# Optimization experiments

Measured on AMD Instinct MI355X. Metric: run time of the kernel, lower is better.

## Reference

```python
import jax, jax.numpy as jnp
import numpy as np

N_SRC, N_TGT, N_EDGES = 100000, 50000, 600000
IN_CH, OUT_CH = 128, 128
NUM_EDGE_TYPES, NUM_NODE_TYPES = 7, 4


def setup_inputs() -> dict:
    key = jax.random.key(0)
    ks = jax.random.split(key, 9)
    x_src = jax.random.normal(ks[0], (N_SRC, IN_CH), dtype=jnp.float32)
    x_target = jax.random.normal(ks[1], (N_TGT, IN_CH), dtype=jnp.float32)
    # PyG Linear: y = x @ W.T (+ b); W has shape (out, in)
    rel_w = jax.random.normal(ks[2], (NUM_EDGE_TYPES, OUT_CH, IN_CH), dtype=jnp.float32) * 0.05
    root_w = jax.random.normal(ks[3], (NUM_NODE_TYPES, OUT_CH, IN_CH), dtype=jnp.float32) * 0.05
    root_b = jax.random.normal(ks[4], (NUM_NODE_TYPES, OUT_CH), dtype=jnp.float32) * 0.05
    edge_src = jax.random.randint(ks[5], (N_EDGES,), 0, N_SRC, dtype=jnp.int32)
    edge_dst = jax.random.randint(ks[6], (N_EDGES,), 0, N_TGT, dtype=jnp.int32)
    edge_type = jax.random.randint(ks[7], (N_EDGES,), 0, NUM_EDGE_TYPES, dtype=jnp.int32)
    target_node_type = jax.random.randint(ks[8], (N_TGT,), 0, NUM_NODE_TYPES, dtype=jnp.int32)
    return {
        "x_src": x_src, "x_target": x_target,
        "rel_w": rel_w, "root_w": root_w, "root_b": root_b,
        "edge_src": edge_src, "edge_dst": edge_dst,
        "edge_type": edge_type, "target_node_type": target_node_type,
    }


def reference(x_src, x_target, rel_w, root_w, root_b,
              edge_src, edge_dst, edge_type, target_node_type):
    n_tgt = x_target.shape[0]
    num_rel = rel_w.shape[0]
    num_ntypes = root_w.shape[0]
    # Gather source features once for all edges: (E, in)
    msg = x_src[edge_src]
    out = jnp.zeros((n_tgt, rel_w.shape[1]), dtype=x_target.dtype)
    # Per-relation linear transform + scatter-MEAN over that relation's edges
    # (matches one propagate(aggr='mean') call per edge type: nodes with no
    #  incoming edges of type r contribute 0 for that relation).
    for r in range(num_rel):
        mask = (edge_type == r).astype(msg.dtype)  # (E,)
        y = (msg * mask[:, None]) @ rel_w[r].T     # (E, out)
        s = jax.ops.segment_sum(y, edge_dst, num_segments=n_tgt)
        cnt = jax.ops.segment_sum(mask, edge_dst, num_segments=n_tgt)
        out = out + s / jnp.maximum(cnt, 1.0)[:, None]
    # Per-node-type root linear (with bias), masked add
    for t in range(num_ntypes):
        m = (target_node_type == t)
        root = x_target @ root_w[t].T + root_b[t]
        out = out + jnp.where(m[:, None], root, 0.0)
    return out
```

## Files before the change

### kernel.cpp

```cpp
#include <hip/hip_runtime.h>

#define NSRC 100000
#define NTGT 50000
#define NE   600000
#define CH   128
#define NREL 7
#define NTYP 4
#define NP   (NREL * NTGT)
#define NB   ((NP + 1023) / 1024)
#define NBLK ((NTGT + 31) / 32)

typedef __attribute__((ext_vector_type(4))) float f32x4;
typedef __attribute__((ext_vector_type(8))) short bf16x8;
typedef unsigned int uint;
typedef unsigned short ushort;

static constexpr long long NXT4 = (long long)NTGT * CH / 4;
static constexpr long long NWR4 = (long long)NREL * CH * CH / 4;
static constexpr long long NWT4 = (long long)NTYP * CH * CH / 4;
static constexpr int CONVB  = (int)((NXT4 + NWR4 + NWT4 + 255) / 256);
static constexpr int COUNTB = (NE + 255) / 256;
static constexpr int GATB   = NE / 16;

static constexpr size_t A256(size_t x) { return (x + 255) & ~(size_t)255; }
static constexpr size_t CNT_O   = 0;
static constexpr size_t BSE_O   = A256(CNT_O + (size_t)NP * 4);
static constexpr size_t EOFF_O  = A256(BSE_O + (size_t)NB * 4);
static constexpr size_t CUR_O   = A256(EOFF_O + (size_t)(NP + 1) * 4);
static constexpr size_t WB_O    = A256(CUR_O + (size_t)NP * 4);
static constexpr size_t XTB_O   = A256(WB_O + (size_t)(NREL + NTYP) * CH * CH * 2);
static constexpr size_t MSG_O   = A256(XTB_O + (size_t)NTGT * CH * 2);

#define GLOAD_LDS(gp, lp) __builtin_amdgcn_global_load_lds( \
    (const __attribute__((address_space(1))) void*)(gp), \
    (__attribute__((address_space(3))) void*)(lp), 16, 0, 0)
#define WAITVM4()   asm volatile("s_waitcnt vmcnt(4)" ::: "memory")
#define WAITVM0()   asm volatile("s_waitcnt vmcnt(0)" ::: "memory")
#define WAITLGKM0() asm volatile("s_waitcnt lgkmcnt(0)" ::: "memory")

__device__ __forceinline__ uint bfpack(float a, float b) {
  uint ua = __float_as_uint(a); ua = (ua + 0x7fff + ((ua >> 16) & 1)) >> 16;
  uint ub = __float_as_uint(b); ub = (ub + 0x7fff + ((ub >> 16) & 1)) >> 16;
  return ua | (ub << 16);
}
__device__ __forceinline__ ushort f2b(float x) {
  uint u = __float_as_uint(x);
  return (ushort)((u + 0x7fff + ((u >> 16) & 1)) >> 16);
}
__device__ __forceinline__ float bl(uint u) { return __uint_as_float(u << 16); }
__device__ __forceinline__ float bh(uint u) { return __uint_as_float(u & 0xffff0000u); }

__global__ __launch_bounds__(256) void k_pre(
    const float* __restrict__ xt, const float* __restrict__ relw,
    const float* __restrict__ rootw, ushort* __restrict__ xtb,
    ushort* __restrict__ wb,
    const int* __restrict__ edst, const int* __restrict__ etyp,
    int* __restrict__ cnt) {
  int bx = blockIdx.x;
  if (bx < CONVB) {
    long long i4 = (long long)bx * 256 + threadIdx.x;
    const float* src; ushort* dst; long long off;
    if (i4 < NXT4) { src = xt; dst = xtb; off = i4; }
    else if (i4 < NXT4 + NWR4) { src = relw; dst = wb; off = i4 - NXT4; }
    else if (i4 < NXT4 + NWR4 + NWT4) {
      src = rootw; dst = wb + (size_t)NREL * CH * CH; off = i4 - NXT4 - NWR4;
    } else return;
    float4 v = *(const float4*)(src + off * 4);
    uint lo = (uint)f2b(v.x) | ((uint)f2b(v.y) << 16);
    uint hi = (uint)f2b(v.z) | ((uint)f2b(v.w) << 16);
    uint2 o = make_uint2(lo, hi);
    *(uint2*)(dst + off * 4) = o;
    return;
  }
  bx -= CONVB;
  int i = bx * 256 + threadIdx.x;
  if (i < NE) atomicAdd(&cnt[etyp[i] * NTGT + edst[i]], 1);
}

__global__ __launch_bounds__(256) void k_s1(const int* __restrict__ cnt,
                                            int* __restrict__ bsE) {
  __shared__ int sE[256];
  int t = threadIdx.x, p0 = blockIdx.x * 1024 + t * 4;
  int e = 0;
#pragma unroll
  for (int j = 0; j < 4; ++j) {
    int p = p0 + j;
    if (p < NP) e += cnt[p];
  }
  sE[t] = e; __syncthreads();
  for (int s = 128; s > 0; s >>= 1) {
    if (t < s) sE[t] += sE[t + s];
    __syncthreads();
  }
  if (t == 0) bsE[blockIdx.x] = sE[0];
}

__global__ __launch_bounds__(512) void k_s23(const int* __restrict__ cnt,
                                             const int* __restrict__ bsE,
                                             int* __restrict__ eoff,
                                             int* __restrict__ cur) {
  __shared__ int sE[512];
  __shared__ int sBase;
  int t = threadIdx.x;
  int e = (t < NB) ? bsE[t] : 0;
  sE[t] = e; __syncthreads();
  for (int s = 1; s < 512; s <<= 1) {
    int a = 0; if (t >= s) a = sE[t - s];
    __syncthreads();
    sE[t] += a;
    __syncthreads();
  }
  if (t == blockIdx.x) sBase = sE[t] - e;
  __syncthreads();
  int base0 = sBase;
  int p0 = blockIdx.x * 1024 + t * 2;
  int c0 = (p0 < NP) ? cnt[p0] : 0;
  int c1 = (p0 + 1 < NP) ? cnt[p0 + 1] : 0;
  int e2 = c0 + c1;
  sE[t] = e2; __syncthreads();
  for (int s = 1; s < 512; s <<= 1) {
    int a = 0; if (t >= s) a = sE[t - s];
    __syncthreads();
    sE[t] += a;
    __syncthreads();
  }
  int baseE = base0 + sE[t] - e2;
  if (p0 < NP)     { eoff[p0] = baseE;          cur[p0] = baseE; }
  if (p0 + 1 < NP) { eoff[p0 + 1] = baseE + c0; cur[p0 + 1] = baseE + c0; }
  if (p0 + 1 == NP - 1) eoff[NP] = baseE + c0 + c1;
}

__global__ __launch_bounds__(256) void k_gat(
    const float* __restrict__ xsrc, const int* __restrict__ esrc,
    const int* __restrict__ edst, const int* __restrict__ etyp,
    int* __restrict__ cur, ushort* __restrict__ msg) {
  int tid = threadIdx.x;
  int e = blockIdx.x * 16 + (tid >> 4);
  int l16 = tid & 15;
  int src = esrc[e];
  int p = etyp[e] * NTGT + edst[e];
  int pos = 0;
  if (l16 == 0) pos = atomicAdd(&cur[p], 1);
  pos = __shfl(pos, (tid & 63) & ~15);
  const float* rp = xsrc + (size_t)src * CH + l16 * 8;
  float4 v0 = *(const float4*)rp;
  float4 v1 = *(const float4*)(rp + 4);
  uint4 o;
  o.x = bfpack(v0.x, v0.y); o.y = bfpack(v0.z, v0.w);
  o.z = bfpack(v1.x, v1.y); o.w = bfpack(v1.z, v1.w);
  *(uint4*)(msg + (size_t)pos * CH + l16 * 8) = o;
}

__device__ __forceinline__ void mfma_acc(const ushort* strip, const ushort* W,
                                         int m, int quad, f32x4* acc) {
  bf16x8 aF[4];
#pragma unroll
  for (int ks = 0; ks < 4; ++ks) {
    int c = ks * 4 + quad;
    aF[ks] = *(const bf16x8*)&strip[(m * 16 + (c ^ m)) << 3];
  }
#pragma unroll
  for (int ct = 0; ct < 8; ++ct) {
    int n = ct * 16 + m;
#pragma unroll
    for (int ks = 0; ks < 4; ++ks) {
      bf16x8 bF = *(const bf16x8*)(W + (size_t)n * CH + ks * 32 + quad * 8);
      acc[ct] = __builtin_amdgcn_mfma_f32_16x16x32_bf16(aF[ks], bF, acc[ct], 0, 0, 0);
    }
  }
}

__global__ __launch_bounds__(128) void k_mega(const ushort* __restrict__ msg,
    const ushort* __restrict__ xtb, const ushort* __restrict__ wb,
    const int* __restrict__ eoff, const int* __restrict__ ntyp,
    const float* __restrict__ rootb, float* __restrict__ out) {
  __shared__ ushort As[2 * 6144];
  int wv = threadIdx.x >> 6, ln = threadIdx.x & 63;
  ushort* Wbuf = As + wv * 6144;
  ushort* strip = Wbuf + 4096;
  int m = ln & 15, quad = ln >> 4;
  int dstbase = blockIdx.x * 32 + wv * 16;
  if (dstbase >= NTGT) return;

  int lc = min(ln, 16);
  int evr[NREL];
#pragma unroll
  for (int r = 0; r < NREL; ++r)
    evr[r] = eoff[r * NTGT + dstbase + lc];

  f32x4 acc[8];
#pragma unroll
  for (int ct = 0; ct < 8; ++ct) acc[ct] = (f32x4){0.f, 0.f, 0.f, 0.f};

#define STAGE(k) do { \
    const ushort* gp = msg + (size_t)(e0 + (k) * 16) * CH + (size_t)(ln * 8); \
    ushort* lb = Wbuf + ((k) & 1) * 2048; \
    GLOAD_LDS(gp, lb); \
    GLOAD_LDS(gp + 4 * CH, lb + 512); \
    GLOAD_LDS(gp + 8 * CH, lb + 1024); \
    GLOAD_LDS(gp + 12 * CH, lb + 1536); \
  } while (0)

  for (int rel = 0; rel < NREL; ++rel) {
    int ev = evr[rel];
    int e0 = __builtin_amdgcn_readlane(ev, 0);
    int e1 = __builtin_amdgcn_readlane(ev, 16);
    if (e1 <= e0) continue;

    float aRx[16], aRy[16];
#pragma unroll
    for (int i = 0; i < 16; ++i) { aRx[i] = 0.f; aRy[i] = 0.f; }

    int nchunk = (e1 - e0 + 15) >> 4;
    WAITLGKM0();
    STAGE(0);
    for (int k = 0; k < nchunk; ++k) {
      if (k + 1 < nchunk) { STAGE(k + 1); WAITVM4(); }
      else               { WAITVM0(); }
      const ushort* buf = Wbuf + (k & 1) * 2048;
      int cb = e0 + k * 16;
      int ce = cb + 16; if (ce > e1) ce = e1;
#pragma unroll
      for (int i = 0; i < 16; ++i) {
        int lo = __builtin_amdgcn_readlane(ev, i);
        int hi = __builtin_amdgcn_readlane(ev, i + 1);
        if (lo < cb) lo = cb;
        if (hi > ce) hi = ce;
        for (int e = lo; e < hi; ++e) {
          uint u = *(const uint*)&buf[((e - cb) << 7) + (ln << 1)];
          aRx[i] += bl(u);
          aRy[i] += bh(u);
        }
      }
    }

#pragma unroll
    for (int i = 0; i < 16; ++i) {
      int n = __builtin_amdgcn_readlane(ev, i + 1) - __builtin_amdgcn_readlane(ev, i);
      float inv = (n > 0) ? __builtin_amdgcn_rcpf((float)n) : 0.f;
      uint w = bfpack(aRx[i] * inv, aRy[i] * inv);
      int c = ln >> 2;
      *(uint*)&strip[((i * 16 + (c ^ i)) << 3) + ((ln & 3) << 1)] = w;
    }
    mfma_acc(strip, wb + (size_t)rel * CH * CH, m, quad, acc);
  }
#undef STAGE

  int nv = ntyp[dstbase + min(ln, 15)];
  uint xr[16];
#pragma unroll
  for (int i = 0; i < 16; ++i)
    xr[i] = *(const uint*)(xtb + (size_t)(dstbase + i) * CH + (ln << 1));
#pragma unroll
  for (int ty = 0; ty < NTYP; ++ty) {
#pragma unroll
    for (int i = 0; i < 16; ++i) {
      int nti = __builtin_amdgcn_readlane(nv, i);
      uint w = (nti == ty) ? xr[i] : 0u;
      int c = ln >> 2;
      *(uint*)&strip[((i * 16 + (c ^ i)) << 3) + ((ln & 3) << 1)] = w;
    }
    mfma_acc(strip, wb + (size_t)(NREL + ty) * CH * CH, m, quad, acc);
  }

#pragma unroll
  for (int reg = 0; reg < 4; ++reg) {
    int row = quad * 4 + reg;
    int dst = dstbase + row;
    int tt = ntyp[dst];
    const float* rb = rootb + (size_t)tt * CH;
#pragma unroll
    for (int ct = 0; ct < 8; ++ct) {
      int col = ct * 16 + m;
      out[(size_t)dst * CH + col] = acc[ct][reg] + rb[col];
    }
  }
}

extern "C" void kernel_launch(void* const* d_in, const int* in_sizes, int n_in,
                              void* d_out, int out_size, void* d_ws, size_t ws_size,
                              hipStream_t stream) {
  (void)in_sizes; (void)n_in; (void)out_size; (void)ws_size;
  const float* xsrc  = (const float*)d_in[0];
  const float* xt    = (const float*)d_in[1];
  const float* relw  = (const float*)d_in[2];
  const float* rootw = (const float*)d_in[3];
  const float* rootb = (const float*)d_in[4];
  const int* esrc = (const int*)d_in[5];
  const int* edst = (const int*)d_in[6];
  const int* etyp = (const int*)d_in[7];
  const int* ntyp = (const int*)d_in[8];
  float* out = (float*)d_out;

  char* ws = (char*)d_ws;
  int*   cnt    = (int*)(ws + CNT_O);
  int*   bsE    = (int*)(ws + BSE_O);
  int*   eoff   = (int*)(ws + EOFF_O);
  int*   cur    = (int*)(ws + CUR_O);
  ushort* wb    = (ushort*)(ws + WB_O);
  ushort* xtb   = (ushort*)(ws + XTB_O);
  ushort* msg   = (ushort*)(ws + MSG_O);

  hipMemsetAsync(cnt, 0, (size_t)NP * 4, stream);
  k_pre<<<dim3(CONVB + COUNTB), dim3(256), 0, stream>>>(
      xt, relw, rootw, xtb, wb, edst, etyp, cnt);
  k_s1<<<dim3(NB), dim3(256), 0, stream>>>(cnt, bsE);
  k_s23<<<dim3(NB), dim3(512), 0, stream>>>(cnt, bsE, eoff, cur);
  k_gat<<<dim3(GATB), dim3(256), 0, stream>>>(xsrc, esrc, edst, etyp, cur, msg);
  k_mega<<<dim3(NBLK), dim3(128), 0, stream>>>(
      msg, xtb, wb, eoff, ntyp, rootb, out);
}
```

Baseline: 383.1 us.

## Segment-sum via MFMA indicator matrix and pre-convert source features to bf16

Replaces the scalar per-row segment reduction in the fused kernel with an MFMA that multiplies a 0/1 indicator matrix by 32-edge chunks staged in padded LDS. A global chunk descriptor list pipelines staging across relations. Blocks shrink to one wave over 16 targets. Source features are converted to bf16 once in the pre-pass so the gather copies half as many bytes, at the cost of an extra full conversion pass over x_src. A zeroed tail pad in msg covers chunk overreads.

```diff
diff --git a/kernel.cpp b/kernel.cpp
--- a/kernel.cpp
+++ b/kernel.cpp
@@ -8,19 +8,26 @@
 #define NTYP 4
 #define NP   (NREL * NTGT)
 #define NB   ((NP + 1023) / 1024)
-#define NBLK ((NTGT + 31) / 32)
+#define NBLK (NTGT / 16)
 
 typedef __attribute__((ext_vector_type(4))) float f32x4;
 typedef __attribute__((ext_vector_type(8))) short bf16x8;
 typedef unsigned int uint;
 typedef unsigned short ushort;
 
+static constexpr long long NXB4 = (long long)NSRC * CH / 4;
 static constexpr long long NXT4 = (long long)NTGT * CH / 4;
 static constexpr long long NWR4 = (long long)NREL * CH * CH / 4;
 static constexpr long long NWT4 = (long long)NTYP * CH * CH / 4;
-static constexpr int CONVB  = (int)((NXT4 + NWR4 + NWT4 + 255) / 256);
+static constexpr int CONVB  = (int)((NXB4 + NXT4 + NWR4 + NWT4 + 255) / 256);
 static constexpr int COUNTB = (NE + 255) / 256;
 static constexpr int GATB   = NE / 16;
+
+#define STRIP_OFF 0
+#define BUF0_OFF  4096
+#define BUFSZB    8320
+#define DESC_OFF  (4096 + 2 * 8320)
+#define LDS_TOT   (DESC_OFF + 2048)
 
 static constexpr size_t A256(size_t x) { return (x + 255) & ~(size_t)255; }
 static constexpr size_t CNT_O   = 0;
@@ -28,42 +35,38 @@
 static constexpr size_t EOFF_O  = A256(BSE_O + (size_t)NB * 4);
 static constexpr size_t CUR_O   = A256(EOFF_O + (size_t)(NP + 1) * 4);
 static constexpr size_t WB_O    = A256(CUR_O + (size_t)NP * 4);
-static constexpr size_t XTB_O   = A256(WB_O + (size_t)(NREL + NTYP) * CH * CH * 2);
+static constexpr size_t XB_O    = A256(WB_O + (size_t)(NREL + NTYP) * CH * CH * 2);
+static constexpr size_t XTB_O   = A256(XB_O + (size_t)NSRC * CH * 2);
 static constexpr size_t MSG_O   = A256(XTB_O + (size_t)NTGT * CH * 2);
 
 #define GLOAD_LDS(gp, lp) __builtin_amdgcn_global_load_lds( \
     (const __attribute__((address_space(1))) void*)(gp), \
     (__attribute__((address_space(3))) void*)(lp), 16, 0, 0)
-#define WAITVM4()   asm volatile("s_waitcnt vmcnt(4)" ::: "memory")
+#define WAITVM8()   asm volatile("s_waitcnt vmcnt(8)" ::: "memory")
 #define WAITVM0()   asm volatile("s_waitcnt vmcnt(0)" ::: "memory")
 #define WAITLGKM0() asm volatile("s_waitcnt lgkmcnt(0)" ::: "memory")
-
-__device__ __forceinline__ uint bfpack(float a, float b) {
-  uint ua = __float_as_uint(a); ua = (ua + 0x7fff + ((ua >> 16) & 1)) >> 16;
-  uint ub = __float_as_uint(b); ub = (ub + 0x7fff + ((ub >> 16) & 1)) >> 16;
-  return ua | (ub << 16);
-}
+#define SB0()       __builtin_amdgcn_sched_barrier(0)
+
 __device__ __forceinline__ ushort f2b(float x) {
   uint u = __float_as_uint(x);
   return (ushort)((u + 0x7fff + ((u >> 16) & 1)) >> 16);
 }
-__device__ __forceinline__ float bl(uint u) { return __uint_as_float(u << 16); }
-__device__ __forceinline__ float bh(uint u) { return __uint_as_float(u & 0xffff0000u); }
 
 __global__ __launch_bounds__(256) void k_pre(
-    const float* __restrict__ xt, const float* __restrict__ relw,
-    const float* __restrict__ rootw, ushort* __restrict__ xtb,
-    ushort* __restrict__ wb,
+    const float* __restrict__ xsrc, const float* __restrict__ xt,
+    const float* __restrict__ relw, const float* __restrict__ rootw,
+    ushort* __restrict__ xb, ushort* __restrict__ xtb, ushort* __restrict__ wb,
     const int* __restrict__ edst, const int* __restrict__ etyp,
     int* __restrict__ cnt) {
   int bx = blockIdx.x;
   if (bx < CONVB) {
     long long i4 = (long long)bx * 256 + threadIdx.x;
     const float* src; ushort* dst; long long off;
-    if (i4 < NXT4) { src = xt; dst = xtb; off = i4; }
-    else if (i4 < NXT4 + NWR4) { src = relw; dst = wb; off = i4 - NXT4; }
-    else if (i4 < NXT4 + NWR4 + NWT4) {
-      src = rootw; dst = wb + (size_t)NREL * CH * CH; off = i4 - NXT4 - NWR4;
+    if (i4 < NXB4) { src = xsrc; dst = xb; off = i4; }
+    else if (i4 < NXB4 + NXT4) { src = xt; dst = xtb; off = i4 - NXB4; }
+    else if (i4 < NXB4 + NXT4 + NWR4) { src = relw; dst = wb; off = i4 - NXB4 - NXT4; }
+    else if (i4 < NXB4 + NXT4 + NWR4 + NWT4) {
+      src = rootw; dst = wb + (size_t)NREL * CH * CH; off = i4 - NXB4 - NXT4 - NWR4;
     } else return;
     float4 v = *(const float4*)(src + off * 4);
     uint lo = (uint)f2b(v.x) | ((uint)f2b(v.y) << 16);
@@ -131,7 +134,7 @@
 }
 
 __global__ __launch_bounds__(256) void k_gat(
-    const float* __restrict__ xsrc, const int* __restrict__ esrc,
+    const ushort* __restrict__ xb, const int* __restrict__ esrc,
     const int* __restrict__ edst, const int* __restrict__ etyp,
     int* __restrict__ cur, ushort* __restrict__ msg) {
   int tid = threadIdx.x;
@@ -142,13 +145,8 @@
   int pos = 0;
   if (l16 == 0) pos = atomicAdd(&cur[p], 1);
   pos = __shfl(pos, (tid & 63) & ~15);
-  const float* rp = xsrc + (size_t)src * CH + l16 * 8;
-  float4 v0 = *(const float4*)rp;
-  float4 v1 = *(const float4*)(rp + 4);
-  uint4 o;
-  o.x = bfpack(v0.x, v0.y); o.y = bfpack(v0.z, v0.w);
-  o.z = bfpack(v1.x, v1.y); o.w = bfpack(v1.z, v1.w);
-  *(uint4*)(msg + (size_t)pos * CH + l16 * 8) = o;
+  uint4 v = *(const uint4*)(xb + (size_t)src * CH + (l16 << 3));
+  *(uint4*)(msg + (size_t)pos * CH + (l16 << 3)) = v;
 }
 
 __device__ __forceinline__ void mfma_acc(const ushort* strip, const ushort* W,
@@ -170,17 +168,16 @@
   }
 }
 
-__global__ __launch_bounds__(128) void k_mega(const ushort* __restrict__ msg,
+__global__ __launch_bounds__(64) void k_mega(const ushort* __restrict__ msg,
     const ushort* __restrict__ xtb, const ushort* __restrict__ wb,
     const int* __restrict__ eoff, const int* __restrict__ ntyp,
     const float* __restrict__ rootb, float* __restrict__ out) {
-  __shared__ ushort As[2 * 6144];
-  int wv = threadIdx.x >> 6, ln = threadIdx.x & 63;
-  ushort* Wbuf = As + wv * 6144;
-  ushort* strip = Wbuf + 4096;
+  __shared__ char As[LDS_TOT];
+  ushort* strip = (ushort*)(As + STRIP_OFF);
+  int* descp = (int*)(As + DESC_OFF);
+  int ln = threadIdx.x;
   int m = ln & 15, quad = ln >> 4;
-  int dstbase = blockIdx.x * 32 + wv * 16;
-  if (dstbase >= NTGT) return;
+  int dstbase = blockIdx.x * 16;
 
   int lc = min(ln, 16);
   int evr[NREL];
@@ -188,60 +185,104 @@
   for (int r = 0; r < NREL; ++r)
     evr[r] = eoff[r * NTGT + dstbase + lc];
 
+  int e0s[NREL], e1s[NREL], crs[NREL];
+  int C = 0;
+#pragma unroll
+  for (int r = 0; r < NREL; ++r) {
+    e0s[r] = __builtin_amdgcn_readlane(evr[r], 0);
+    e1s[r] = __builtin_amdgcn_readlane(evr[r], 16);
+    crs[r] = (e1s[r] - e0s[r] + 31) >> 5;
+  }
+#pragma unroll
+  for (int r = 0; r < NREL; ++r) {
+    for (int c = 0; c < crs[r]; ++c) {
+      if (ln == 0) descp[C + c] = e0s[r] + c * 32;
+    }
+    C += crs[r];
+  }
+
   f32x4 acc[8];
 #pragma unroll
   for (int ct = 0; ct < 8; ++ct) acc[ct] = (f32x4){0.f, 0.f, 0.f, 0.f};
 
-#define STAGE(k) do { \
-    const ushort* gp = msg + (size_t)(e0 + (k) * 16) * CH + (size_t)(ln * 8); \
-    ushort* lb = Wbuf + ((k) & 1) * 2048; \
-    GLOAD_LDS(gp, lb); \
-    GLOAD_LDS(gp + 4 * CH, lb + 512); \
-    GLOAD_LDS(gp + 8 * CH, lb + 1024); \
-    GLOAD_LDS(gp + 12 * CH, lb + 1536); \
-  } while (0)
-
+#define STAGE(bufoff, estart) do { \
+    _Pragma("unroll") \
+    for (int g = 0; g < 8; ++g) { \
+      const ushort* gp = msg + (size_t)((estart) + g * 4 + quad) * CH + (m << 3); \
+      GLOAD_LDS(gp, As + (bufoff) + g * 1040); \
+    } } while (0)
+
+  int tstg = 0, tcons = 0;
+  if (C > 0) {
+    int d0 = descp[0];
+    WAITLGKM0();
+    SB0();
+    STAGE(BUF0_OFF, d0);
+    tstg = 1;
+  }
+
+#pragma unroll
   for (int rel = 0; rel < NREL; ++rel) {
-    int ev = evr[rel];
-    int e0 = __builtin_amdgcn_readlane(ev, 0);
-    int e1 = __builtin_amdgcn_readlane(ev, 16);
-    if (e1 <= e0) continue;
-
-    float aRx[16], aRy[16];
-#pragma unroll
-    for (int i = 0; i < 16; ++i) { aRx[i] = 0.f; aRy[i] = 0.f; }
-
-    int nchunk = (e1 - e0 + 15) >> 4;
+    if (crs[rel] == 0) continue;
+    int lo_m = __shfl(evr[rel], m);
+    int hi_m = __shfl(evr[rel], m + 1);
+
+    f32x4 seg[8];
+#pragma unroll
+    for (int ct = 0; ct < 8; ++ct) seg[ct] = (f32x4){0.f, 0.f, 0.f, 0.f};
+
+    for (int c = 0; c < crs[rel]; ++c) {
+      if (tstg < C) {
+        int nd = descp[tstg];
+        WAITLGKM0();
+        SB0();
+        STAGE(BUF0_OFF + (tstg & 1) * BUFSZB, nd);
+        ++tstg;
+      }
+      if (tstg > tcons + 1) { WAITVM8(); } else { WAITVM0(); }
+      SB0();
+      const char* buf = As + BUF0_OFF + (tcons & 1) * BUFSZB;
+      int cb = e0s[rel] + c * 32;
+      int k0 = lo_m - cb, k1 = hi_m - cb;
+
+      union { uint u[4]; bf16x8 v; } Afr;
+      int kq = quad * 8;
+#pragma unroll
+      for (int p2 = 0; p2 < 4; ++p2) {
+        int kk = kq + p2 * 2;
+        uint lo = (kk >= k0 && kk < k1) ? 0x3f80u : 0u;
+        uint hi = (kk + 1 >= k0 && kk + 1 < k1) ? 0x3f800000u : 0u;
+        Afr.u[p2] = lo | hi;
+      }
+#pragma unroll
+      for (int ct = 0; ct < 8; ++ct) {
+        union { ushort s[8]; bf16x8 v; } Bfr;
+#pragma unroll
+        for (int j = 0; j < 8; ++j) {
+          int e = kq + j;
+          Bfr.s[j] = *(const ushort*)(buf + e * 256 + ((e >> 2) << 4) +
+                                      ((ct * 16 + m) << 1));
+        }
+        seg[ct] = __builtin_amdgcn_mfma_f32_16x16x32_bf16(Afr.v, Bfr.v, seg[ct], 0, 0, 0);
+      }
+      ++tcons;
+    }
+
+#pragma unroll
+    for (int reg = 0; reg < 4; ++reg) {
+      int row = quad * 4 + reg;
+      int lo = __shfl(evr[rel], row);
+      int hi = __shfl(evr[rel], row + 1);
+      float inv = (hi > lo) ? __builtin_amdgcn_rcpf((float)(hi - lo)) : 0.f;
+#pragma unroll
+      for (int ct = 0; ct < 8; ++ct) {
+        int ch = ct * 16 + m;
+        int cblk = ch >> 3;
+        strip[((row * 16 + (cblk ^ row)) << 3) + (ch & 7)] = f2b(seg[ct][reg] * inv);
+      }
+    }
     WAITLGKM0();
-    STAGE(0);
-    for (int k = 0; k < nchunk; ++k) {
-      if (k + 1 < nchunk) { STAGE(k + 1); WAITVM4(); }
-      else               { WAITVM0(); }
-      const ushort* buf = Wbuf + (k & 1) * 2048;
-      int cb = e0 + k * 16;
-      int ce = cb + 16; if (ce > e1) ce = e1;
-#pragma unroll
-      for (int i = 0; i < 16; ++i) {
-        int lo = __builtin_amdgcn_readlane(ev, i);
-        int hi = __builtin_amdgcn_readlane(ev, i + 1);
-        if (lo < cb) lo = cb;
-        if (hi > ce) hi = ce;
-        for (int e = lo; e < hi; ++e) {
-          uint u = *(const uint*)&buf[((e - cb) << 7) + (ln << 1)];
-          aRx[i] += bl(u);
-          aRy[i] += bh(u);
-        }
-      }
-    }
-
-#pragma unroll
-    for (int i = 0; i < 16; ++i) {
-      int n = __builtin_amdgcn_readlane(ev, i + 1) - __builtin_amdgcn_readlane(ev, i);
-      float inv = (n > 0) ? __builtin_amdgcn_rcpf((float)n) : 0.f;
-      uint w = bfpack(aRx[i] * inv, aRy[i] * inv);
-      int c = ln >> 2;
-      *(uint*)&strip[((i * 16 + (c ^ i)) << 3) + ((ln & 3) << 1)] = w;
-    }
+    SB0();
     mfma_acc(strip, wb + (size_t)rel * CH * CH, m, quad, acc);
   }
 #undef STAGE
@@ -257,9 +298,11 @@
     for (int i = 0; i < 16; ++i) {
       int nti = __builtin_amdgcn_readlane(nv, i);
       uint w = (nti == ty) ? xr[i] : 0u;
-      int c = ln >> 2;
-      *(uint*)&strip[((i * 16 + (c ^ i)) << 3) + ((ln & 3) << 1)] = w;
-    }
+      int cb2 = ln >> 2;
+      *(uint*)&strip[((i * 16 + (cb2 ^ i)) << 3) + ((ln & 3) << 1)] = w;
+    }
+    WAITLGKM0();
+    SB0();
     mfma_acc(strip, wb + (size_t)(NREL + ty) * CH * CH, m, quad, acc);
   }
 
@@ -298,15 +341,17 @@
   int*   eoff   = (int*)(ws + EOFF_O);
   int*   cur    = (int*)(ws + CUR_O);
   ushort* wb    = (ushort*)(ws + WB_O);
+  ushort* xb    = (ushort*)(ws + XB_O);
   ushort* xtb   = (ushort*)(ws + XTB_O);
   ushort* msg   = (ushort*)(ws + MSG_O);
 
   hipMemsetAsync(cnt, 0, (size_t)NP * 4, stream);
+  hipMemsetAsync(msg + (size_t)NE * CH, 0, (size_t)32 * CH * 2, stream);
   k_pre<<<dim3(CONVB + COUNTB), dim3(256), 0, stream>>>(
-      xt, relw, rootw, xtb, wb, edst, etyp, cnt);
+      xsrc, xt, relw, rootw, xb, xtb, wb, edst, etyp, cnt);
   k_s1<<<dim3(NB), dim3(256), 0, stream>>>(cnt, bsE);
   k_s23<<<dim3(NB), dim3(512), 0, stream>>>(cnt, bsE, eoff, cur);
-  k_gat<<<dim3(GATB), dim3(256), 0, stream>>>(xsrc, esrc, edst, etyp, cur, msg);
-  k_mega<<<dim3(NBLK), dim3(128), 0, stream>>>(
+  k_gat<<<dim3(GATB), dim3(256), 0, stream>>>(xb, esrc, edst, etyp, cur, msg);
+  k_mega<<<dim3(NBLK), dim3(64), 0, stream>>>(
       msg, xtb, wb, eoff, ntyp, rootb, out);
 }
```

New measurement: 381.1 us. No clear change (-0.5%).
